# Kernel optimization log

Measured on AMD Instinct MI355X. Metric: run time of the kernel, lower is better.

The kernel has to match this reference:

```python
import jax, jax.numpy as jnp
import numpy as np

N_NODES = 100000
N_EDGES = 1600000
IN_CH = 64
HID = 64
OUT_CH = 16


def setup_inputs() -> dict:
    key = jax.random.key(0)
    ks = jax.random.split(key, 8)
    x = jax.random.normal(ks[0], (N_NODES, IN_CH), dtype=jnp.float32)
    edge_index = jax.random.randint(ks[1], (2, N_EDGES), 0, N_NODES, dtype=jnp.int64)
    s = 1.0 / np.sqrt(IN_CH)
    W1l = jax.random.normal(ks[2], (HID, IN_CH), dtype=jnp.float32) * s
    W1r = jax.random.normal(ks[3], (HID, IN_CH), dtype=jnp.float32) * s
    b1 = jnp.zeros((HID,), dtype=jnp.float32)
    W2l = jax.random.normal(ks[4], (HID, HID), dtype=jnp.float32) * s
    W2r = jax.random.normal(ks[5], (HID, HID), dtype=jnp.float32) * s
    b2 = jnp.zeros((HID,), dtype=jnp.float32)
    Wlin = jax.random.normal(ks[6], (OUT_CH, HID), dtype=jnp.float32) * s
    blin = jnp.zeros((OUT_CH,), dtype=jnp.float32)
    return {"x": x, "edge_index": edge_index, "W1l": W1l, "b1": b1, "W1r": W1r,
            "W2l": W2l, "b2": b2, "W2r": W2r, "Wlin": Wlin, "blin": blin}


def _sage_conv(x, src, dst, Wl, b, Wr):
    # PyG SAGEConv with mean aggregation:
    # out = lin_l(mean_{j in N(i)} x_j) + lin_r(x_i); bias lives in lin_l.
    msgs = x[src]                                              # [E, F] gather
    summed = jax.ops.segment_sum(msgs, dst, num_segments=N_NODES)  # [N, F]
    cnt = jax.ops.segment_sum(jnp.ones((src.shape[0],), x.dtype), dst,
                              num_segments=N_NODES)            # [N]
    agg = summed / jnp.maximum(cnt, 1.0)[:, None]              # mean, deg-0 safe
    return agg @ Wl.T + b + x @ Wr.T


def reference(x, edge_index, W1l, b1, W1r, W2l, b2, W2r, Wlin, blin):
    src, dst = edge_index[0], edge_index[1]
    h = jax.nn.relu(_sage_conv(x, src, dst, W1l, b1, W1r))
    h = jax.nn.relu(_sage_conv(h, src, dst, W2l, b2, W2r))
    return h @ Wlin.T + blin
```

## Files before the change

### kernel.cpp

```cpp
#include <hip/hip_runtime.h>

#define NN 100000
#define NE 1600000

#define BSHIFT 9
#define BWIDTH 512
#define NBUCK 196
#define SLOTS 12288
#define CHUNK 4096
#define B1_BLOCKS ((NE + CHUNK - 1) / CHUNK)
#define GEMM_BLOCKS ((NN + 63) / 64)
#define AGG_CAP 1024

typedef float    v2f __attribute__((ext_vector_type(2)));
typedef unsigned v2u __attribute__((ext_vector_type(2)));
typedef short    bf16x8 __attribute__((ext_vector_type(8)));
typedef float    f32x4  __attribute__((ext_vector_type(4)));

__device__ __forceinline__ float u2f(unsigned u) {
    union { unsigned u; float f; } v; v.u = u; return v.f;
}
__device__ __forceinline__ unsigned f2u(float f) {
    union { float f; unsigned u; } v; v.f = f; return v.u;
}
__device__ __forceinline__ unsigned f2bf(float f) {
    unsigned u = f2u(f);
    return (u + 0x7FFFu + ((u >> 16) & 1u)) >> 16;
}
__device__ __forceinline__ v2f unpk(unsigned x) {
    v2u w; w[0] = x << 16; w[1] = x & 0xFFFF0000u;
    union { v2u u; v2f f; } c; c.u = w; return c.f;
}
__device__ __forceinline__ int wave_incl_scan(int v, int lane) {
    #pragma unroll
    for (int off = 1; off < 64; off <<= 1) {
        int u = __shfl_up(v, off);
        if (lane >= off) v += u;
    }
    return v;
}

__global__ void detect_mode_kernel(const int* ei32, int* flag, int* bcnt) {
    __shared__ int any_nonzero;
    if (threadIdx.x == 0) any_nonzero = 0;
    if (threadIdx.x < NBUCK) bcnt[threadIdx.x] = 0;
    __syncthreads();
    int idx = 1 + 2 * threadIdx.x;
    if (ei32[idx] != 0) atomicOr(&any_nonzero, 1);
    __syncthreads();
    if (threadIdx.x == 0) flag[0] = (any_nonzero == 0) ? 1 : 0;
}

__device__ __forceinline__ void load_edge(const void* ei, int is64, int e,
                                          int& s, int& d) {
    if (is64) {
        const long long* p = (const long long*)ei;
        s = (int)p[e];
        d = (int)p[NE + e];
    } else {
        const int* p = (const int*)ei;
        s = p[e];
        d = p[NE + e];
    }
}

template<int BF16IN>
__device__ __forceinline__ void gemm_mfma_body(
    char* smem, const void* __restrict__ featv,
    const float* __restrict__ Wl, const float* __restrict__ Wr,
    const float* __restrict__ bias,
    unsigned* __restrict__ outt, unsigned* __restrict__ outr,
    int tile, int t)
{
    unsigned short* Als = (unsigned short*)smem;
    unsigned short* Bls = (unsigned short*)(smem + 9216);
    const int lane = t & 63, w = t >> 6;
    const int m0 = tile * 64;
    const float*    featf = (const float*)featv;
    const unsigned* featu = (const unsigned*)featv;

    #pragma unroll
    for (int rep = 0; rep < 2; ++rep) {
        int task = t + 256 * rep;
        int row = task >> 3, s = task & 7;
        int gn = m0 + row;
        uint4 u;
        if (BF16IN) {
            u = (gn < NN) ? *(const uint4*)(featu + (size_t)gn * 32 + 4 * s)
                          : make_uint4(0u, 0u, 0u, 0u);
        } else {
            if (gn < NN) {
                float4 v0 = *(const float4*)(featf + (size_t)gn * 64 + 8 * s);
                float4 v1 = *(const float4*)(featf + (size_t)gn * 64 + 8 * s + 4);
                u.x = f2bf(v0.x) | (f2bf(v0.y) << 16);
                u.y = f2bf(v0.z) | (f2bf(v0.w) << 16);
                u.z = f2bf(v1.x) | (f2bf(v1.y) << 16);
                u.w = f2bf(v1.z) | (f2bf(v1.w) << 16);
            } else u = make_uint4(0u, 0u, 0u, 0u);
        }
        *(uint4*)(Als + row * 72 + 8 * s) = u;
    }
    #pragma unroll
    for (int rep = 0; rep < 4; ++rep) {
        int task = t + 256 * rep;
        int c = task >> 3, s = task & 7;
        const float* Wsrc = (c < 64) ? (Wl + (size_t)c * 64)
                                     : (Wr + (size_t)(c - 64) * 64);
        float4 v0 = *(const float4*)(Wsrc + 8 * s);
        float4 v1 = *(const float4*)(Wsrc + 8 * s + 4);
        uint4 u;
        u.x = f2bf(v0.x) | (f2bf(v0.y) << 16);
        u.y = f2bf(v0.z) | (f2bf(v0.w) << 16);
        u.z = f2bf(v1.x) | (f2bf(v1.y) << 16);
        u.w = f2bf(v1.z) | (f2bf(v1.w) << 16);
        *(uint4*)(Bls + c * 72 + 8 * s) = u;
    }
    __syncthreads();

    const int r = lane & 15, g = lane >> 4;
    const int cw0 = 32 * w;

    bf16x8 bf[2][2];
    #pragma unroll
    for (int ct = 0; ct < 2; ++ct)
        #pragma unroll
        for (int ks = 0; ks < 2; ++ks) {
            int c = cw0 + 16 * ct + r;
            bf[ct][ks] = *(const bf16x8*)(Bls + c * 72 + (ks * 4 + g) * 8);
        }

    f32x4 acc[4][2];
    #pragma unroll
    for (int nt = 0; nt < 4; ++nt)
        #pragma unroll
        for (int ct = 0; ct < 2; ++ct)
            acc[nt][ct] = (f32x4){0.f, 0.f, 0.f, 0.f};

    #pragma unroll
    for (int nt = 0; nt < 4; ++nt) {
        bf16x8 af[2];
        #pragma unroll
        for (int ks = 0; ks < 2; ++ks) {
            int rr = nt * 16 + r;
            af[ks] = *(const bf16x8*)(Als + rr * 72 + (ks * 4 + g) * 8);
        }
        #pragma unroll
        for (int ct = 0; ct < 2; ++ct)
            #pragma unroll
            for (int ks = 0; ks < 2; ++ks)
                acc[nt][ct] = __builtin_amdgcn_mfma_f32_16x16x32_bf16(
                    af[ks], bf[ct][ks], acc[nt][ct], 0, 0, 0);
    }

    unsigned short* Tb = (unsigned short*)outt;
    unsigned short* Rb = (unsigned short*)outr;
    #pragma unroll
    for (int ct = 0; ct < 2; ++ct) {
        int c = cw0 + 16 * ct + r;
        float badd = (c >= 64) ? bias[c - 64] : 0.f;
        unsigned short* dst = (c < 64) ? (Tb + c) : (Rb + (c - 64));
        #pragma unroll
        for (int nt = 0; nt < 4; ++nt)
            #pragma unroll
            for (int i = 0; i < 4; ++i) {
                int row = m0 + nt * 16 + g * 4 + i;
                if (row < NN)
                    dst[(size_t)row * 64] = (unsigned short)f2bf(acc[nt][ct][i] + badd);
            }
    }
}

__global__ __launch_bounds__(256) void b1_gemm1_kernel(
    const void* ei, const int* flag,
    int* __restrict__ bcnt, int* __restrict__ bpk,
    const float* __restrict__ x,
    const float* __restrict__ W1l, const float* __restrict__ W1r,
    const float* __restrict__ b1,
    unsigned* __restrict__ T, unsigned* __restrict__ R)
{
    __shared__ __align__(16) char smem[27648];
    const int t = threadIdx.x;

    if (blockIdx.x >= B1_BLOCKS) {
        if (blockIdx.x == B1_BLOCKS && t < 32) T[(size_t)NN * 32 + t] = 0u;
        gemm_mfma_body<0>(smem, x, W1l, W1r, b1, T, R, blockIdx.x - B1_BLOCKS, t);
        return;
    }

    int* stage = (int*)smem;
    unsigned char* sbuck = (unsigned char*)(smem + 16384);
    int* hist  = (int*)(smem + 20480);
    int* scanb = (int*)(smem + 21264);
    int* gbase = (int*)(smem + 22048);
    int* lofs  = (int*)(smem + 22832);
    int* wsum  = (int*)(smem + 23616);

    const int is64 = *flag;
    const int e0 = blockIdx.x * CHUNK;
    const int nE = min(CHUNK, NE - e0);
    const int lane = t & 63, wvi = t >> 6;

    for (int i = t; i < NBUCK; i += 256) { hist[i] = 0; lofs[i] = 0; }
    __syncthreads();

    int sr[16], dr[16];
    #pragma unroll
    for (int rr = 0; rr < 16; ++rr) {
        int e = e0 + t + 256 * rr;
        if (e < NE) load_edge(ei, is64, e, sr[rr], dr[rr]);
        else dr[rr] = -1;
    }
    #pragma unroll
    for (int rr = 0; rr < 16; ++rr)
        if (dr[rr] >= 0) atomicAdd(&hist[dr[rr] >> BSHIFT], 1);
    __syncthreads();

    int v = (t < NBUCK) ? hist[t] : 0;
    int s = wave_incl_scan(v, lane);
    if (lane == 63) wsum[wvi] = s;
    __syncthreads();
    int add = 0;
    #pragma unroll
    for (int k = 0; k < 3; ++k) if (wvi > k) add += wsum[k];
    s += add;
    if (t < NBUCK) {
        scanb[t] = s - v;
        gbase[t] = atomicAdd(&bcnt[t], v);
    }
    __syncthreads();

    #pragma unroll
    for (int rr = 0; rr < 16; ++rr) {
        if (dr[rr] >= 0) {
            int b = dr[rr] >> BSHIFT;
            int p = scanb[b] + atomicAdd(&lofs[b], 1);
            stage[p] = (sr[rr] << BSHIFT) | (dr[rr] & (BWIDTH - 1));
            sbuck[p] = (unsigned char)b;
        }
    }
    __syncthreads();

    for (int i = t; i < nE; i += 256) {
        int b = sbuck[i];
        int off = gbase[b] + (i - scanb[b]);
        if (off < SLOTS) bpk[(size_t)b * SLOTS + off] = stage[i];
    }
}

__global__ __launch_bounds__(512) void bucket_to_csr_kernel(
    const int* __restrict__ bcnt, const int* __restrict__ bpk,
    int* __restrict__ rowptr, int* __restrict__ colb)
{
    __shared__ int ldeg[512], lptr[512], lcnt[512], sc[512], wsum[8];
    const int t = threadIdx.x, b = blockIdx.x;
    const int lane = t & 63, wvi = t >> 6;

    int v = (t < NBUCK) ? bcnt[t] : 0;
    int s = wave_incl_scan(v, lane);
    if (lane == 63) wsum[wvi] = s;
    __syncthreads();
    int add = 0;
    #pragma unroll
    for (int k = 0; k < 7; ++k) if (wvi > k) add += wsum[k];
    s += add;
    sc[t] = s;
    __syncthreads();
    const int base = (b == 0) ? 0 : sc[b - 1];
    if (b == 0 && t == 0) rowptr[NN] = NE;
    __syncthreads();

    ldeg[t] = 0; lcnt[t] = 0;
    __syncthreads();

    const int n0 = b << BSHIFT;
    const int cnt = min(bcnt[b], SLOTS);
    const int* src = bpk + (size_t)b * SLOTS;
    for (int i = t; i < cnt; i += 512)
        atomicAdd(&ldeg[src[i] & (BWIDTH - 1)], 1);
    __syncthreads();

    int a = ldeg[t];
    int s2 = wave_incl_scan(a, lane);
    if (lane == 63) wsum[wvi] = s2;
    __syncthreads();
    int add2 = 0;
    #pragma unroll
    for (int k = 0; k < 7; ++k) if (wvi > k) add2 += wsum[k];
    s2 += add2;
    lptr[t] = s2 - a;
    __syncthreads();

    int gn = n0 + t;
    if (gn < NN) rowptr[gn] = base + lptr[t];

    for (int i = t; i < cnt; i += 512) {
        int p = src[i];
        int li = p & (BWIDTH - 1);
        int pos = lptr[li] + atomicAdd(&lcnt[li], 1);
        colb[base + pos] = (p >> BSHIFT) << 7;
    }
}

__global__ __launch_bounds__(256) void gemm2_kernel(
    const unsigned* __restrict__ feat,
    const float* __restrict__ Wl, const float* __restrict__ Wr,
    const float* __restrict__ bias,
    unsigned* __restrict__ outt, unsigned* __restrict__ outr)
{
    __shared__ __align__(16) char smem[27648];
    gemm_mfma_body<1>(smem, feat, Wl, Wr, bias, outt, outr, blockIdx.x, threadIdx.x);
}

#define AGG_STEP(O0, O1, O2, O3)                                              \
    {                                                                         \
        int o0 = O0, o1 = O1, o2 = O2, o3 = O3;                               \
        o0 = (jj      < end) ? o0 : zoff;                                     \
        o1 = (jj + 4  < end) ? o1 : zoff;                                     \
        o2 = (jj + 8  < end) ? o2 : zoff;                                     \
        o3 = (jj + 12 < end) ? o3 : zoff;                                     \
        uint4 u0 = *(const uint4*)(tb + (size_t)(unsigned)o0 + 16 * c8);      \
        uint4 u1 = *(const uint4*)(tb + (size_t)(unsigned)o1 + 16 * c8);      \
        uint4 u2 = *(const uint4*)(tb + (size_t)(unsigned)o2 + 16 * c8);      \
        uint4 u3 = *(const uint4*)(tb + (size_t)(unsigned)o3 + 16 * c8);      \
        a0 += unpk(u0.x); a1 += unpk(u0.y); a2 += unpk(u0.z); a3 += unpk(u0.w);\
        b0 += unpk(u1.x); b1 += unpk(u1.y); b2 += unpk(u1.z); b3 += unpk(u1.w);\
        a0 += unpk(u2.x); a1 += unpk(u2.y); a2 += unpk(u2.z); a3 += unpk(u2.w);\
        b0 += unpk(u3.x); b1 += unpk(u3.y); b2 += unpk(u3.z); b3 += unpk(u3.w);\
    }

template<int FINAL>
__global__ void aggregate_relu_kernel(const int* __restrict__ rowptr,
                                      const int* __restrict__ colb,
                                      const unsigned* __restrict__ tt,
                                      unsigned* rh,
                                      const float* __restrict__ Wlin,
                                      const float* __restrict__ blin,
                                      float* __restrict__ out) {
    __shared__ int lcol[AGG_CAP];
    __shared__ float wls[16 * 68];
    __shared__ unsigned short hbuf[8][72];
    const int t = threadIdx.x;
    const int n0 = blockIdx.x * 8;
    const int lane = t & 63;
    const int w = t >> 6;
    const int half = lane >> 5;
    const int slot = (lane >> 3) & 3;
    const int c8   = lane & 7;
    const int node = n0 + 2 * w + half;

    const int cbeg  = rowptr[n0];
    const int cendB = rowptr[min(n0 + 8, NN)];
    const int total = cendB - cbeg;
    const bool fast = (total <= AGG_CAP);
    if (fast) {
        for (int i = t; i < total; i += 256) lcol[i] = colb[cbeg + i];
    }
    if (FINAL) {
        for (int i = t; i < 1024; i += 256) {
            int cc = i >> 6, k = i & 63;
            wls[cc * 68 + k] = Wlin[i];
        }
    }
    __syncthreads();

    const int beg = rowptr[node], end = rowptr[node + 1];
    const int deg = end - beg;
    int niter = (deg + 3) >> 2;
    niter = max(niter, __shfl_xor(niter, 32));

    const char* tb = (const char*)tt;
    const int zoff = NN * 128;
    v2f a0 = {0.f, 0.f}, a1 = {0.f, 0.f}, a2 = {0.f, 0.f}, a3 = {0.f, 0.f};
    v2f b0 = {0.f, 0.f}, b1 = {0.f, 0.f}, b2 = {0.f, 0.f}, b3 = {0.f, 0.f};

    int jj = beg + slot;
    int it = 0;
    if (fast) {
        for (; it + 4 <= niter; it += 4, jj += 16) {
            int jc0 = min(jj,      end - 1) - cbeg;
            int jc1 = min(jj + 4,  end - 1) - cbeg;
            int jc2 = min(jj + 8,  end - 1) - cbeg;
            int jc3 = min(jj + 12, end - 1) - cbeg;
            AGG_STEP(lcol[jc0], lcol[jc1], lcol[jc2], lcol[jc3])
        }
        for (; it < niter; ++it, jj += 4) {
            int jc0 = min(jj, end - 1) - cbeg;
            int o0 = lcol[jc0];
            o0 = (jj < end) ? o0 : zoff;
            uint4 u0 = *(const uint4*)(tb + (size_t)(unsigned)o0 + 16 * c8);
            a0 += unpk(u0.x); a1 += unpk(u0.y); a2 += unpk(u0.z); a3 += unpk(u0.w);
        }
    } else {
        for (; it + 4 <= niter; it += 4, jj += 16) {
            int jc0 = min(jj,      end - 1);
            int jc1 = min(jj + 4,  end - 1);
            int jc2 = min(jj + 8,  end - 1);
            int jc3 = min(jj + 12, end - 1);
            AGG_STEP(colb[jc0], colb[jc1], colb[jc2], colb[jc3])
        }
        for (; it < niter; ++it, jj += 4) {
            int jc0 = min(jj, end - 1);
            int o0 = colb[jc0];
            o0 = (jj < end) ? o0 : zoff;
            uint4 u0 = *(const uint4*)(tb + (size_t)(unsigned)o0 + 16 * c8);
            a0 += unpk(u0.x); a1 += unpk(u0.y); a2 += unpk(u0.z); a3 += unpk(u0.w);
        }
    }
    a0 += b0; a1 += b1; a2 += b2; a3 += b3;

    a0[0] += __shfl_xor(a0[0], 8);  a0[1] += __shfl_xor(a0[1], 8);
    a1[0] += __shfl_xor(a1[0], 8);  a1[1] += __shfl_xor(a1[1], 8);
    a2[0] += __shfl_xor(a2[0], 8);  a2[1] += __shfl_xor(a2[1], 8);
    a3[0] += __shfl_xor(a3[0], 8);  a3[1] += __shfl_xor(a3[1], 8);
    a0[0] += __shfl_xor(a0[0], 16); a0[1] += __shfl_xor(a0[1], 16);
    a1[0] += __shfl_xor(a1[0], 16); a1[1] += __shfl_xor(a1[1], 16);
    a2[0] += __shfl_xor(a2[0], 16); a2[1] += __shfl_xor(a2[1], 16);
    a3[0] += __shfl_xor(a3[0], 16); a3[1] += __shfl_xor(a3[1], 16);

    if (slot == 0) {
        float inv = 1.0f / fmaxf((float)deg, 1.0f);
        unsigned* p = rh + (size_t)node * 32 + 4 * c8;
        uint4 rr = *(const uint4*)p;
        v2f q0 = unpk(rr.x), q1 = unpk(rr.y), q2 = unpk(rr.z), q3 = unpk(rr.w);
        float h0 = fmaxf(fmaf(a0[0], inv, q0[0]), 0.0f);
        float h1 = fmaxf(fmaf(a0[1], inv, q0[1]), 0.0f);
        float h2 = fmaxf(fmaf(a1[0], inv, q1[0]), 0.0f);
        float h3 = fmaxf(fmaf(a1[1], inv, q1[1]), 0.0f);
        float h4 = fmaxf(fmaf(a2[0], inv, q2[0]), 0.0f);
        float h5 = fmaxf(fmaf(a2[1], inv, q2[1]), 0.0f);
        float h6 = fmaxf(fmaf(a3[0], inv, q3[0]), 0.0f);
        float h7 = fmaxf(fmaf(a3[1], inv, q3[1]), 0.0f);
        uint4 wv4;
        wv4.x = f2bf(h0) | (f2bf(h1) << 16);
        wv4.y = f2bf(h2) | (f2bf(h3) << 16);
        wv4.z = f2bf(h4) | (f2bf(h5) << 16);
        wv4.w = f2bf(h6) | (f2bf(h7) << 16);
        if (FINAL) {
            *(uint4*)&hbuf[2 * w + half][8 * c8] = wv4;
        } else {
            *(uint4*)p = wv4;
        }
    }

    if (FINAL) {
        __syncthreads();
        if (t < 128) {
            int i = t >> 4, cc = t & 15;
            int gnode = n0 + i;
            const unsigned* hrow = (const unsigned*)hbuf[i];
            float acc = blin[cc];
            #pragma unroll
            for (int k2 = 0; k2 < 32; ++k2) {
                v2f hv = unpk(hrow[k2]);
                acc = fmaf(hv[0], wls[cc * 68 + 2 * k2], acc);
                acc = fmaf(hv[1], wls[cc * 68 + 2 * k2 + 1], acc);
            }
            if (gnode < NN)
                out[(size_t)gnode * 16 + cc] = acc;
        }
    }
}

extern "C" void kernel_launch(void* const* d_in, const int* in_sizes, int n_in,
                              void* d_out, int out_size, void* d_ws, size_t ws_size,
                              hipStream_t stream) {
    const float* x    = (const float*)d_in[0];
    const void*  ei   = d_in[1];
    const float* W1l  = (const float*)d_in[2];
    const float* b1   = (const float*)d_in[3];
    const float* W1r  = (const float*)d_in[4];
    const float* W2l  = (const float*)d_in[5];
    const float* b2   = (const float*)d_in[6];
    const float* W2r  = (const float*)d_in[7];
    const float* Wlin = (const float*)d_in[8];
    const float* blin = (const float*)d_in[9];
    float* out = (float*)d_out;

    char* w = (char*)d_ws;
    int*      flag   = (int*)w;
    int*      bcnt   = (int*)(w + (size_t)4 * 1024);
    int*      rowptr = (int*)(w + (size_t)1024 * 1024);
    int*      colb   = (int*)(w + (size_t)2 * 1024 * 1024);
    int*      bpk    = (int*)(w + (size_t)10 * 1024 * 1024);
    unsigned* T      = (unsigned*)(w + (size_t)30 * 1024 * 1024);
    unsigned* R      = (unsigned*)(w + (size_t)43 * 1024 * 1024);

    detect_mode_kernel<<<1, 256, 0, stream>>>((const int*)ei, flag, bcnt);

    b1_gemm1_kernel<<<B1_BLOCKS + GEMM_BLOCKS, 256, 0, stream>>>(
        ei, flag, bcnt, bpk, x, W1l, W1r, b1, T, R);

    bucket_to_csr_kernel<<<NBUCK, 512, 0, stream>>>(bcnt, bpk, rowptr, colb);

    const int aggBlocks = (NN + 7) / 8;

    aggregate_relu_kernel<0><<<aggBlocks, 256, 0, stream>>>(
        rowptr, colb, T, R, nullptr, nullptr, nullptr);

    gemm2_kernel<<<GEMM_BLOCKS, 256, 0, stream>>>(R, W2l, W2r, b2, T, R);

    aggregate_relu_kernel<1><<<aggBlocks, 256, 0, stream>>>(
        rowptr, colb, T, R, Wlin, blin, out);
}
```

Measured before the change: 145.3 us.

## Fuse layer-1 aggregation with layer-2 GEMM in one kernel

Replaces the separate layer-1 aggregate kernel and gemm2 kernel with one kernel. Each block aggregates 64 nodes into LDS as bf16 and then runs the MFMA GEMM on that tile. This avoids a global write and re-read of the hidden features and one kernel launch. Because the layer-1 T buffer is still being read by other blocks, the layer-2 transformed features go to a separate buffer T2 placed over the bucket scratch area. The cost is fewer blocks (64 nodes each, 8 rounds of serial aggregation), which lowers gather parallelism and occupancy.

```diff
diff --git a/kernel.cpp b/kernel.cpp
--- a/kernel.cpp
+++ b/kernel.cpp
@@ -11,6 +11,7 @@
 #define B1_BLOCKS ((NE + CHUNK - 1) / CHUNK)
 #define GEMM_BLOCKS ((NN + 63) / 64)
 #define AGG_CAP 1024
+#define FUSE_CAP 2048
 
 typedef float    v2f __attribute__((ext_vector_type(2)));
 typedef unsigned v2u __attribute__((ext_vector_type(2)));
@@ -64,9 +65,8 @@
     }
 }
 
-template<int BF16IN>
-__device__ __forceinline__ void gemm_mfma_body(
-    char* smem, const void* __restrict__ featv,
+__device__ __forceinline__ void gemm_mfma_body_f32(
+    char* smem, const float* __restrict__ featf,
     const float* __restrict__ Wl, const float* __restrict__ Wr,
     const float* __restrict__ bias,
     unsigned* __restrict__ outt, unsigned* __restrict__ outr,
@@ -76,8 +76,6 @@
     unsigned short* Bls = (unsigned short*)(smem + 9216);
     const int lane = t & 63, w = t >> 6;
     const int m0 = tile * 64;
-    const float*    featf = (const float*)featv;
-    const unsigned* featu = (const unsigned*)featv;
 
     #pragma unroll
     for (int rep = 0; rep < 2; ++rep) {
@@ -85,19 +83,14 @@
         int row = task >> 3, s = task & 7;
         int gn = m0 + row;
         uint4 u;
-        if (BF16IN) {
-            u = (gn < NN) ? *(const uint4*)(featu + (size_t)gn * 32 + 4 * s)
-                          : make_uint4(0u, 0u, 0u, 0u);
-        } else {
-            if (gn < NN) {
-                float4 v0 = *(const float4*)(featf + (size_t)gn * 64 + 8 * s);
-                float4 v1 = *(const float4*)(featf + (size_t)gn * 64 + 8 * s + 4);
-                u.x = f2bf(v0.x) | (f2bf(v0.y) << 16);
-                u.y = f2bf(v0.z) | (f2bf(v0.w) << 16);
-                u.z = f2bf(v1.x) | (f2bf(v1.y) << 16);
-                u.w = f2bf(v1.z) | (f2bf(v1.w) << 16);
-            } else u = make_uint4(0u, 0u, 0u, 0u);
-        }
+        if (gn < NN) {
+            float4 v0 = *(const float4*)(featf + (size_t)gn * 64 + 8 * s);
+            float4 v1 = *(const float4*)(featf + (size_t)gn * 64 + 8 * s + 4);
+            u.x = f2bf(v0.x) | (f2bf(v0.y) << 16);
+            u.y = f2bf(v0.z) | (f2bf(v0.w) << 16);
+            u.z = f2bf(v1.x) | (f2bf(v1.y) << 16);
+            u.w = f2bf(v1.z) | (f2bf(v1.w) << 16);
+        } else u = make_uint4(0u, 0u, 0u, 0u);
         *(uint4*)(Als + row * 72 + 8 * s) = u;
     }
     #pragma unroll
@@ -140,10 +133,8 @@
     for (int nt = 0; nt < 4; ++nt) {
         bf16x8 af[2];
         #pragma unroll
-        for (int ks = 0; ks < 2; ++ks) {
-            int rr = nt * 16 + r;
-            af[ks] = *(const bf16x8*)(Als + rr * 72 + (ks * 4 + g) * 8);
-        }
+        for (int ks = 0; ks < 2; ++ks)
+            af[ks] = *(const bf16x8*)(Als + (nt * 16 + r) * 72 + (ks * 4 + g) * 8);
         #pragma unroll
         for (int ct = 0; ct < 2; ++ct)
             #pragma unroll
@@ -183,7 +174,7 @@
 
     if (blockIdx.x >= B1_BLOCKS) {
         if (blockIdx.x == B1_BLOCKS && t < 32) T[(size_t)NN * 32 + t] = 0u;
-        gemm_mfma_body<0>(smem, x, W1l, W1r, b1, T, R, blockIdx.x - B1_BLOCKS, t);
+        gemm_mfma_body_f32(smem, x, W1l, W1r, b1, T, R, blockIdx.x - B1_BLOCKS, t);
         return;
     }
 
@@ -299,16 +290,6 @@
         int pos = lptr[li] + atomicAdd(&lcnt[li], 1);
         colb[base + pos] = (p >> BSHIFT) << 7;
     }
-}
-
-__global__ __launch_bounds__(256) void gemm2_kernel(
-    const unsigned* __restrict__ feat,
-    const float* __restrict__ Wl, const float* __restrict__ Wr,
-    const float* __restrict__ bias,
-    unsigned* __restrict__ outt, unsigned* __restrict__ outr)
-{
-    __shared__ __align__(16) char smem[27648];
-    gemm_mfma_body<1>(smem, feat, Wl, Wr, bias, outt, outr, blockIdx.x, threadIdx.x);
 }
 
 #define AGG_STEP(O0, O1, O2, O3)                                              \
@@ -328,11 +309,193 @@
         b0 += unpk(u3.x); b1 += unpk(u3.y); b2 += unpk(u3.z); b3 += unpk(u3.w);\
     }
 
-template<int FINAL>
-__global__ void aggregate_relu_kernel(const int* __restrict__ rowptr,
+__global__ __launch_bounds__(256) void agg1_gemm2_kernel(
+    const int* __restrict__ rowptr, const int* __restrict__ colb,
+    const unsigned* __restrict__ tt,
+    unsigned* __restrict__ rh,
+    const float* __restrict__ W2l, const float* __restrict__ W2r,
+    const float* __restrict__ b2,
+    unsigned* __restrict__ outt2)
+{
+    __shared__ __align__(16) char smem[36864];
+    unsigned short* Als = (unsigned short*)smem;
+    unsigned short* Bls = (unsigned short*)(smem + 9216);
+    int* lcol = (int*)(smem + 9216 + 18432);
+
+    const int t = threadIdx.x;
+    const int lane = t & 63, w = t >> 6;
+    const int m0 = blockIdx.x * 64;
+
+    if (blockIdx.x == 0 && t < 32) outt2[(size_t)NN * 32 + t] = 0u;
+
+    #pragma unroll
+    for (int rep = 0; rep < 4; ++rep) {
+        int task = t + 256 * rep;
+        int c = task >> 3, s = task & 7;
+        const float* Wsrc = (c < 64) ? (W2l + (size_t)c * 64)
+                                     : (W2r + (size_t)(c - 64) * 64);
+        float4 v0 = *(const float4*)(Wsrc + 8 * s);
+        float4 v1 = *(const float4*)(Wsrc + 8 * s + 4);
+        uint4 u;
+        u.x = f2bf(v0.x) | (f2bf(v0.y) << 16);
+        u.y = f2bf(v0.z) | (f2bf(v0.w) << 16);
+        u.z = f2bf(v1.x) | (f2bf(v1.y) << 16);
+        u.w = f2bf(v1.z) | (f2bf(v1.w) << 16);
+        *(uint4*)(Bls + c * 72 + 8 * s) = u;
+    }
+
+    const int nend = min(m0 + 64, NN);
+    const int cbeg = rowptr[m0];
+    const int cendB = rowptr[nend];
+    const int total = cendB - cbeg;
+    const bool fast = (total <= FUSE_CAP);
+    if (fast) {
+        for (int i = t; i < total; i += 256) lcol[i] = colb[cbeg + i];
+    }
+    __syncthreads();
+
+    const int half = lane >> 5;
+    const int slot = (lane >> 3) & 3;
+    const int c8   = lane & 7;
+    const char* tb = (const char*)tt;
+    const int zoff = NN * 128;
+
+    #pragma unroll 1
+    for (int rnd = 0; rnd < 8; ++rnd) {
+        const int row = rnd * 8 + 2 * w + half;
+        const int node = m0 + row;
+        int beg = 0, end = 0;
+        if (node < NN) { beg = rowptr[node]; end = rowptr[node + 1]; }
+        const int deg = end - beg;
+        int niter = (deg + 3) >> 2;
+        niter = max(niter, __shfl_xor(niter, 32));
+
+        v2f a0 = {0.f, 0.f}, a1 = {0.f, 0.f}, a2 = {0.f, 0.f}, a3 = {0.f, 0.f};
+        v2f b0 = {0.f, 0.f}, b1 = {0.f, 0.f}, b2v = {0.f, 0.f}, b3 = {0.f, 0.f};
+        #define b2 b2v
+        int jj = beg + slot;
+        int it = 0;
+        if (fast) {
+            for (; it + 4 <= niter; it += 4, jj += 16) {
+                int jc0 = min(jj,      end - 1) - cbeg;
+                int jc1 = min(jj + 4,  end - 1) - cbeg;
+                int jc2 = min(jj + 8,  end - 1) - cbeg;
+                int jc3 = min(jj + 12, end - 1) - cbeg;
+                AGG_STEP(lcol[jc0], lcol[jc1], lcol[jc2], lcol[jc3])
+            }
+            for (; it < niter; ++it, jj += 4) {
+                int jc0 = min(jj, end - 1) - cbeg;
+                int o0 = lcol[jc0];
+                o0 = (jj < end) ? o0 : zoff;
+                uint4 u0 = *(const uint4*)(tb + (size_t)(unsigned)o0 + 16 * c8);
+                a0 += unpk(u0.x); a1 += unpk(u0.y); a2 += unpk(u0.z); a3 += unpk(u0.w);
+            }
+        } else {
+            for (; it + 4 <= niter; it += 4, jj += 16) {
+                int jc0 = min(jj,      end - 1);
+                int jc1 = min(jj + 4,  end - 1);
+                int jc2 = min(jj + 8,  end - 1);
+                int jc3 = min(jj + 12, end - 1);
+                AGG_STEP(colb[jc0], colb[jc1], colb[jc2], colb[jc3])
+            }
+            for (; it < niter; ++it, jj += 4) {
+                int jc0 = min(jj, end - 1);
+                int o0 = colb[jc0];
+                o0 = (jj < end) ? o0 : zoff;
+                uint4 u0 = *(const uint4*)(tb + (size_t)(unsigned)o0 + 16 * c8);
+                a0 += unpk(u0.x); a1 += unpk(u0.y); a2 += unpk(u0.z); a3 += unpk(u0.w);
+            }
+        }
+        #undef b2
+        a0 += b0; a1 += b1; a2 += b2v; a3 += b3;
+
+        a0[0] += __shfl_xor(a0[0], 8);  a0[1] += __shfl_xor(a0[1], 8);
+        a1[0] += __shfl_xor(a1[0], 8);  a1[1] += __shfl_xor(a1[1], 8);
+        a2[0] += __shfl_xor(a2[0], 8);  a2[1] += __shfl_xor(a2[1], 8);
+        a3[0] += __shfl_xor(a3[0], 8);  a3[1] += __shfl_xor(a3[1], 8);
+        a0[0] += __shfl_xor(a0[0], 16); a0[1] += __shfl_xor(a0[1], 16);
+        a1[0] += __shfl_xor(a1[0], 16); a1[1] += __shfl_xor(a1[1], 16);
+        a2[0] += __shfl_xor(a2[0], 16); a2[1] += __shfl_xor(a2[1], 16);
+        a3[0] += __shfl_xor(a3[0], 16); a3[1] += __shfl_xor(a3[1], 16);
+
+        if (slot == 0 && node < NN) {
+            float inv = 1.0f / fmaxf((float)deg, 1.0f);
+            const unsigned* p = rh + (size_t)node * 32 + 4 * c8;
+            uint4 rr = *(const uint4*)p;
+            v2f q0 = unpk(rr.x), q1 = unpk(rr.y), q2 = unpk(rr.z), q3 = unpk(rr.w);
+            float h0 = fmaxf(fmaf(a0[0], inv, q0[0]), 0.0f);
+            float h1 = fmaxf(fmaf(a0[1], inv, q0[1]), 0.0f);
+            float h2 = fmaxf(fmaf(a1[0], inv, q1[0]), 0.0f);
+            float h3 = fmaxf(fmaf(a1[1], inv, q1[1]), 0.0f);
+            float h4 = fmaxf(fmaf(a2[0], inv, q2[0]), 0.0f);
+            float h5 = fmaxf(fmaf(a2[1], inv, q2[1]), 0.0f);
+            float h6 = fmaxf(fmaf(a3[0], inv, q3[0]), 0.0f);
+            float h7 = fmaxf(fmaf(a3[1], inv, q3[1]), 0.0f);
+            uint4 wv4;
+            wv4.x = f2bf(h0) | (f2bf(h1) << 16);
+            wv4.y = f2bf(h2) | (f2bf(h3) << 16);
+            wv4.z = f2bf(h4) | (f2bf(h5) << 16);
+            wv4.w = f2bf(h6) | (f2bf(h7) << 16);
+            *(uint4*)(Als + row * 72 + 8 * c8) = wv4;
+        }
+    }
+    __syncthreads();
+
+    const int r = lane & 15, g = lane >> 4;
+    const int cw0 = 32 * w;
+
+    bf16x8 bf[2][2];
+    #pragma unroll
+    for (int ct = 0; ct < 2; ++ct)
+        #pragma unroll
+        for (int ks = 0; ks < 2; ++ks) {
+            int c = cw0 + 16 * ct + r;
+            bf[ct][ks] = *(const bf16x8*)(Bls + c * 72 + (ks * 4 + g) * 8);
+        }
+
+    f32x4 acc[4][2];
+    #pragma unroll
+    for (int nt = 0; nt < 4; ++nt)
+        #pragma unroll
+        for (int ct = 0; ct < 2; ++ct)
+            acc[nt][ct] = (f32x4){0.f, 0.f, 0.f, 0.f};
+
+    #pragma unroll
+    for (int nt = 0; nt < 4; ++nt) {
+        bf16x8 af[2];
+        #pragma unroll
+        for (int ks = 0; ks < 2; ++ks)
+            af[ks] = *(const bf16x8*)(Als + (nt * 16 + r) * 72 + (ks * 4 + g) * 8);
+        #pragma unroll
+        for (int ct = 0; ct < 2; ++ct)
+            #pragma unroll
+            for (int ks = 0; ks < 2; ++ks)
+                acc[nt][ct] = __builtin_amdgcn_mfma_f32_16x16x32_bf16(
+                    af[ks], bf[ct][ks], acc[nt][ct], 0, 0, 0);
+    }
+
+    unsigned short* Tb = (unsigned short*)outt2;
+    unsigned short* Rb = (unsigned short*)rh;
+    #pragma unroll
+    for (int ct = 0; ct < 2; ++ct) {
+        int c = cw0 + 16 * ct + r;
+        float badd = (c >= 64) ? b2[c - 64] : 0.f;
+        unsigned short* dst = (c < 64) ? (Tb + c) : (Rb + (c - 64));
+        #pragma unroll
+        for (int nt = 0; nt < 4; ++nt)
+            #pragma unroll
+            for (int i = 0; i < 4; ++i) {
+                int row = m0 + nt * 16 + g * 4 + i;
+                if (row < NN)
+                    dst[(size_t)row * 64] = (unsigned short)f2bf(acc[nt][ct][i] + badd);
+            }
+    }
+}
+
+__global__ void aggregate_head_kernel(const int* __restrict__ rowptr,
                                       const int* __restrict__ colb,
                                       const unsigned* __restrict__ tt,
-                                      unsigned* rh,
+                                      const unsigned* __restrict__ rh,
                                       const float* __restrict__ Wlin,
                                       const float* __restrict__ blin,
                                       float* __restrict__ out) {
@@ -355,11 +518,9 @@
     if (fast) {
         for (int i = t; i < total; i += 256) lcol[i] = colb[cbeg + i];
     }
-    if (FINAL) {
-        for (int i = t; i < 1024; i += 256) {
-            int cc = i >> 6, k = i & 63;
-            wls[cc * 68 + k] = Wlin[i];
-        }
+    for (int i = t; i < 1024; i += 256) {
+        int cc = i >> 6, k = i & 63;
+        wls[cc * 68 + k] = Wlin[i];
     }
     __syncthreads();
 
@@ -419,7 +580,7 @@
 
     if (slot == 0) {
         float inv = 1.0f / fmaxf((float)deg, 1.0f);
-        unsigned* p = rh + (size_t)node * 32 + 4 * c8;
+        const unsigned* p = rh + (size_t)node * 32 + 4 * c8;
         uint4 rr = *(const uint4*)p;
         v2f q0 = unpk(rr.x), q1 = unpk(rr.y), q2 = unpk(rr.z), q3 = unpk(rr.w);
         float h0 = fmaxf(fmaf(a0[0], inv, q0[0]), 0.0f);
@@ -435,29 +596,23 @@
         wv4.y = f2bf(h2) | (f2bf(h3) << 16);
         wv4.z = f2bf(h4) | (f2bf(h5) << 16);
         wv4.w = f2bf(h6) | (f2bf(h7) << 16);
-        if (FINAL) {
-            *(uint4*)&hbuf[2 * w + half][8 * c8] = wv4;
-        } else {
-            *(uint4*)p = wv4;
-        }
-    }
-
-    if (FINAL) {
-        __syncthreads();
-        if (t < 128) {
-            int i = t >> 4, cc = t & 15;
-            int gnode = n0 + i;
-            const unsigned* hrow = (const unsigned*)hbuf[i];
-            float acc = blin[cc];
-            #pragma unroll
-            for (int k2 = 0; k2 < 32; ++k2) {
-                v2f hv = unpk(hrow[k2]);
-                acc = fmaf(hv[0], wls[cc * 68 + 2 * k2], acc);
-                acc = fmaf(hv[1], wls[cc * 68 + 2 * k2 + 1], acc);
-            }
-            if (gnode < NN)
-                out[(size_t)gnode * 16 + cc] = acc;
-        }
+        *(uint4*)&hbuf[2 * w + half][8 * c8] = wv4;
+    }
+    __syncthreads();
+
+    if (t < 128) {
+        int i = t >> 4, cc = t & 15;
+        int gnode = n0 + i;
+        const unsigned* hrow = (const unsigned*)hbuf[i];
+        float acc = blin[cc];
+        #pragma unroll
+        for (int k2 = 0; k2 < 32; ++k2) {
+            v2f hv = unpk(hrow[k2]);
+            acc = fmaf(hv[0], wls[cc * 68 + 2 * k2], acc);
+            acc = fmaf(hv[1], wls[cc * 68 + 2 * k2 + 1], acc);
+        }
+        if (gnode < NN)
+            out[(size_t)gnode * 16 + cc] = acc;
     }
 }
 
@@ -482,6 +637,7 @@
     int*      rowptr = (int*)(w + (size_t)1024 * 1024);
     int*      colb   = (int*)(w + (size_t)2 * 1024 * 1024);
     int*      bpk    = (int*)(w + (size_t)10 * 1024 * 1024);
+    unsigned* T2     = (unsigned*)(w + (size_t)10 * 1024 * 1024);
     unsigned* T      = (unsigned*)(w + (size_t)30 * 1024 * 1024);
     unsigned* R      = (unsigned*)(w + (size_t)43 * 1024 * 1024);
 
@@ -492,13 +648,10 @@
 
     bucket_to_csr_kernel<<<NBUCK, 512, 0, stream>>>(bcnt, bpk, rowptr, colb);
 
+    agg1_gemm2_kernel<<<GEMM_BLOCKS, 256, 0, stream>>>(
+        rowptr, colb, T, R, W2l, W2r, b2, T2);
+
     const int aggBlocks = (NN + 7) / 8;
-
-    aggregate_relu_kernel<0><<<aggBlocks, 256, 0, stream>>>(
-        rowptr, colb, T, R, nullptr, nullptr, nullptr);
-
-    gemm2_kernel<<<GEMM_BLOCKS, 256, 0, stream>>>(R, W2l, W2r, b2, T, R);
-
-    aggregate_relu_kernel<1><<<aggBlocks, 256, 0, stream>>>(
-        rowptr, colb, T, R, Wlin, blin, out);
-}
+    aggregate_head_kernel<<<aggBlocks, 256, 0, stream>>>(
+        rowptr, colb, T2, R, Wlin, blin, out);
+}
```

Measured after the change: 146.6 us. About the same (+0.9%).
